# Performance work log

Measured on AMD Instinct MI355X. Metric: run time of the kernel, lower is better.

## Reference

```python
import jax, jax.numpy as jnp
import numpy as np


def setup_inputs() -> dict:
    key = jax.random.key(0)
    k1, k2, k3, k4 = jax.random.split(key, 4)
    B, D_vis, E, N = 512, 4096, 1024, 512
    vf = jax.random.normal(k1, (B, D_vis), dtype=jnp.float32)
    p_lfs = jax.random.normal(k2, (B, E), dtype=jnp.float32)
    n_lfs = jax.random.normal(k3, (N, E), dtype=jnp.float32)
    W = jax.random.normal(k4, (E, D_vis), dtype=jnp.float32) * (1.0 / np.sqrt(D_vis))
    b = jnp.zeros((E,), dtype=jnp.float32)
    return {"vf": vf, "p_lfs": p_lfs, "n_lfs": n_lfs, "W": W, "b": b}


def _partial_order_sim(hypers, hypos):
    # -||relu(hypers - hypos)||_2 along last dim
    act = jax.nn.relu(hypers - hypos)
    return -jnp.sqrt(jnp.sum(act * act, axis=-1))


def reference(vf, p_lfs, n_lfs, W, b):
    # vf: [B, D_vis], W: [E, D_vis] -> vf_emb: [B, E]
    vf_emb = jnp.einsum("bd,ed->be", vf, W) + b
    # positive scores: [B]
    p_scores = _partial_order_sim(p_lfs, vf_emb)
    # negative scores, batched over B: n_lfs [N,E] vs vf_emb [B,E] -> [B,N]
    n_scores = _partial_order_sim(n_lfs[None, :, :], vf_emb[:, None, :])
    # score_stack: [B, 1+N]
    return jnp.concatenate([p_scores[:, None], n_scores], axis=1)
```

## Files before the change

### kernel.cpp

```cpp
#include <hip/hip_runtime.h>
#include <hip/hip_bf16.h>

constexpr int B = 512;
constexpr int D = 4096;
constexpr int E = 1024;
constexpr int N = 512;
constexpr int KS = 8;
constexpr int KC = D / KS;
constexpr int NSTEP = KC / 32;
constexpr int ES = 8;
constexpr int EC = E / ES;
constexpr int DEPTH = 4;

typedef __attribute__((ext_vector_type(8))) short bf16x8;
typedef __attribute__((ext_vector_type(4))) float f32x4;
typedef _Float16 h2 __attribute__((ext_vector_type(2)));
typedef _Float16 h4 __attribute__((ext_vector_type(4)));
typedef _Float16 h8 __attribute__((ext_vector_type(8)));

typedef __attribute__((address_space(3))) void lds_void;
typedef const __attribute__((address_space(1))) void gbl_void;

__device__ __forceinline__ unsigned short f2bf(float f) {
    __hip_bfloat16 h = __float2bfloat16(f);
    return *reinterpret_cast<unsigned short*>(&h);
}

#if __has_builtin(__builtin_amdgcn_fdot2)
__device__ __forceinline__ float fdot2(h2 a, h2 b, float c) {
    return __builtin_amdgcn_fdot2(a, b, c, false);
}
#else
__device__ __forceinline__ float fdot2(h2 a, h2 b, float c) {
    return c + (float)a[0] * (float)b[0] + (float)a[1] * (float)b[1];
}
#endif

__global__ __launch_bounds__(256) void cvt_all(
    const float* __restrict__ vf, const float* __restrict__ W,
    const float* __restrict__ n_lfs,
    unsigned short* __restrict__ vfB, unsigned short* __restrict__ WB,
    _Float16* __restrict__ n16)
{
    const int bid = blockIdx.x;
    if (bid < 3072) {
        const float* src;
        unsigned short* dst;
        int i;
        if (bid < 1024) { src = vf; dst = vfB; i = (bid * 256 + threadIdx.x) * 8; }
        else           { src = W;  dst = WB;  i = ((bid - 1024) * 256 + threadIdx.x) * 8; }
        float4 v0 = *(const float4*)(src + i);
        float4 v1 = *(const float4*)(src + i + 4);
        bf16x8 o;
        o[0] = (short)f2bf(v0.x); o[1] = (short)f2bf(v0.y);
        o[2] = (short)f2bf(v0.z); o[3] = (short)f2bf(v0.w);
        o[4] = (short)f2bf(v1.x); o[5] = (short)f2bf(v1.y);
        o[6] = (short)f2bf(v1.z); o[7] = (short)f2bf(v1.w);
        *(bf16x8*)(dst + i) = o;
    } else {
        const int i = ((bid - 3072) * 256 + threadIdx.x) * 8;
        float4 v0 = *(const float4*)(n_lfs + i);
        float4 v1 = *(const float4*)(n_lfs + i + 4);
        h8 o;
        o[0] = (_Float16)v0.x; o[1] = (_Float16)v0.y;
        o[2] = (_Float16)v0.z; o[3] = (_Float16)v0.w;
        o[4] = (_Float16)v1.x; o[5] = (_Float16)v1.y;
        o[6] = (_Float16)v1.z; o[7] = (_Float16)v1.w;
        *(h8*)(n16 + i) = o;
    }
}

__global__ __launch_bounds__(64) void gemm_lds(
    const unsigned short* __restrict__ vf,
    const unsigned short* __restrict__ W,
    float* __restrict__ part)
{
    __shared__ __align__(16) char smem[32768];

    const int L  = threadIdx.x;

    const int id = blockIdx.x + 16 * blockIdx.y + 128 * blockIdx.z;
    const int l  = (id & 7) * 128 + (id >> 3);
    const int ks = l >> 7;
    const int n0 = (l & 15) * 64;
    const int m0 = ((l >> 4) & 7) * 64;

    const int subrow = L >> 2;
    const int qstg = (L & 3) ^ ((L >> 2) & 3) ^ ((L >> 4) & 3);
    const int kbeg = ks * KC;
    const unsigned short* aSrc[4];
    const unsigned short* bSrc[4];
    #pragma unroll
    for (int c = 0; c < 4; ++c) {
        aSrc[c] = vf + (size_t)(m0 + c * 16 + subrow) * D + kbeg + qstg * 8;
        bSrc[c] = W  + (size_t)(n0 + c * 16 + subrow) * D + kbeg + qstg * 8;
    }

    const int r16 = L & 15;
    const int quad = L >> 4;
    const int swz = quad ^ (r16 & 3) ^ ((r16 >> 2) & 3);
    const int aoff = r16 * 64 + swz * 16;

    f32x4 acc[4][4] = {};

    auto issue = [&](int step, int buf) {
        const size_t koff = (size_t)step * 32;
        #pragma unroll
        for (int c = 0; c < 4; ++c) {
            __builtin_amdgcn_global_load_lds(
                (gbl_void*)(aSrc[c] + koff),
                (lds_void*)(smem + buf * 4096 + c * 1024), 16, 0, 0);
            __builtin_amdgcn_global_load_lds(
                (gbl_void*)(bSrc[c] + koff),
                (lds_void*)(smem + 16384 + buf * 4096 + c * 1024), 16, 0, 0);
        }
    };

    issue(0, 0);
    issue(1, 1);
    issue(2, 2);
    issue(3, 3);

    #define GSTEP(S, WC, ISS)                                                  \
    {                                                                          \
        const int buf_ = (S) & 3;                                              \
        __builtin_amdgcn_s_waitcnt(WC);                                        \
        bf16x8 af[4], bg[4];                                                   \
        _Pragma("unroll")                                                      \
        for (int i = 0; i < 4; ++i)                                            \
            af[i] = *(const bf16x8*)(smem + buf_ * 4096 + i * 1024 + aoff);    \
        _Pragma("unroll")                                                      \
        for (int j = 0; j < 4; ++j)                                            \
            bg[j] = *(const bf16x8*)(smem + 16384 + buf_ * 4096 + j * 1024 + aoff); \
        _Pragma("unroll")                                                      \
        for (int i = 0; i < 4; ++i)                                            \
            _Pragma("unroll")                                                  \
            for (int j = 0; j < 4; ++j)                                        \
                acc[i][j] = __builtin_amdgcn_mfma_f32_16x16x32_bf16(           \
                    af[i], bg[j], acc[i][j], 0, 0, 0);                         \
        if (ISS) issue((S) + DEPTH, buf_);                                     \
    }

    #pragma unroll 1
    for (int s = 0; s < NSTEP - DEPTH; ++s)
        GSTEP(s, 0x4F78, true);
    GSTEP(NSTEP - 4, 0x4F78, false);
    GSTEP(NSTEP - 3, 0x4F70, false);
    GSTEP(NSTEP - 2, 0x0F78, false);
    GSTEP(NSTEP - 1, 0x0F70, false);
    #undef GSTEP

    float* ct = (float*)smem;
    #pragma unroll
    for (int i = 0; i < 4; ++i)
        #pragma unroll
        for (int j = 0; j < 4; ++j)
            #pragma unroll
            for (int r = 0; r < 4; ++r)
                ct[(i * 16 + quad * 4 + r) * 69 + (j * 16 + r16)] = acc[i][j][r];
    __builtin_amdgcn_s_waitcnt(0xC07F);
    __builtin_amdgcn_sched_barrier(0);
    float* po = part + (size_t)ks * B * E + (size_t)(m0 + L) * E + n0;
    const float* crow = ct + L * 69;
    #pragma unroll
    for (int c4 = 0; c4 < 16; ++c4) {
        f32x4 v;
        v[0] = crow[c4 * 4];     v[1] = crow[c4 * 4 + 1];
        v[2] = crow[c4 * 4 + 2]; v[3] = crow[c4 * 4 + 3];
        *(f32x4*)(po + c4 * 4) = v;
    }
}

__global__ __launch_bounds__(256) void reduce_emb(
    const float* __restrict__ part, const float* __restrict__ bias,
    const float* __restrict__ p_lfs,
    _Float16* __restrict__ emb16, float* __restrict__ out)
{
    const int b = blockIdx.x;
    const int e = threadIdx.x * 4;
    const size_t base = (size_t)b * E + e;
    float4 s = *(const float4*)(bias + e);
    #pragma unroll
    for (int ks = 0; ks < KS; ++ks) {
        float4 p = *(const float4*)(part + (size_t)ks * B * E + base);
        s.x += p.x; s.y += p.y; s.z += p.z; s.w += p.w;
    }
    h4 o;
    o[0] = (_Float16)s.x; o[1] = (_Float16)s.y;
    o[2] = (_Float16)s.z; o[3] = (_Float16)s.w;
    *(h4*)(emb16 + base) = o;

    const float4 pl = *(const float4*)(p_lfs + base);
    float d, a = 0.f;
    d = pl.x - s.x; d = fmaxf(d, 0.f); a = fmaf(d, d, a);
    d = pl.y - s.y; d = fmaxf(d, 0.f); a = fmaf(d, d, a);
    d = pl.z - s.z; d = fmaxf(d, 0.f); a = fmaf(d, d, a);
    d = pl.w - s.w; d = fmaxf(d, 0.f); a = fmaf(d, d, a);
    #pragma unroll
    for (int off = 32; off; off >>= 1) a += __shfl_down(a, off, 64);
    __shared__ float red[4];
    if ((threadIdx.x & 63) == 0) red[threadIdx.x >> 6] = a;
    __syncthreads();
    if (threadIdx.x == 0)
        out[(size_t)b * 513] = -sqrtf(red[0] + red[1] + red[2] + red[3]);
}

__global__ __launch_bounds__(256, 4) void scores_part(
    const _Float16* __restrict__ emb16,
    const _Float16* __restrict__ n16,
    float* __restrict__ pn)
{
    constexpr int LDH = EC + 8;
    __shared__ _Float16 eS[64 * LDH];
    __shared__ _Float16 nS[64 * LDH];

    const int t  = threadIdx.x;
    const int n0 = blockIdx.x * 64;
    const int b0 = blockIdx.y * 64;
    const int e0 = blockIdx.z * EC;

    {
        const int row = t >> 2;
        const int cb  = (t & 3) * 32;
        const _Float16* ep = emb16 + (size_t)(b0 + row) * E + e0 + cb;
        const _Float16* np = n16   + (size_t)(n0 + row) * E + e0 + cb;
        _Float16* ed = &eS[row * LDH + cb];
        _Float16* nd = &nS[row * LDH + cb];
        #pragma unroll
        for (int q = 0; q < 4; ++q) {
            h8 v = *(const h8*)(ep + q * 8);
            h8 w = *(const h8*)(np + q * 8);
            *(h8*)(ed + q * 8) = -v;
            *(h8*)(nd + q * 8) = w;
        }
    }
    __syncthreads();

    const int ty = t >> 4;
    const int tx = t & 15;

    float acc[4][4] = {};
    const h4 z4 = {};

    #pragma unroll 2
    for (int e = 0; e < EC; e += 4) {
        h4 a[4], c[4];
        #pragma unroll
        for (int r = 0; r < 4; ++r)
            a[r] = *(const h4*)&eS[(ty + 16 * r) * LDH + e];
        #pragma unroll
        for (int q = 0; q < 4; ++q)
            c[q] = *(const h4*)&nS[(tx + 16 * q) * LDH + e];
        #pragma unroll
        for (int r = 0; r < 4; ++r)
            #pragma unroll
            for (int q = 0; q < 4; ++q) {
                h4 d = c[q] + a[r];
                d = __builtin_elementwise_max(d, z4);
                h2 dl = __builtin_shufflevector(d, d, 0, 1);
                h2 dh = __builtin_shufflevector(d, d, 2, 3);
                acc[r][q] = fdot2(dl, dl, acc[r][q]);
                acc[r][q] = fdot2(dh, dh, acc[r][q]);
            }
    }

    float* po = pn + (size_t)blockIdx.z * B * N;
    #pragma unroll
    for (int r = 0; r < 4; ++r) {
        const size_t ob = (size_t)(b0 + ty + 16 * r) * N;
        #pragma unroll
        for (int q = 0; q < 4; ++q)
            po[ob + n0 + tx + 16 * q] = acc[r][q];
    }
}

__global__ __launch_bounds__(256) void scores_final(
    const float* __restrict__ pn,
    float* __restrict__ out)
{
    const int i = blockIdx.x * 256 + threadIdx.x;
    const int b = i >> 9;
    const int n = i & (N - 1);
    float s = 0.f;
    #pragma unroll
    for (int z = 0; z < ES; ++z)
        s += pn[(size_t)z * B * N + i];
    out[(size_t)b * 513 + 1 + n] = -sqrtf(s);
}

extern "C" void kernel_launch(void* const* d_in, const int* in_sizes, int n_in,
                              void* d_out, int out_size, void* d_ws, size_t ws_size,
                              hipStream_t stream) {
    const float* vf    = (const float*)d_in[0];
    const float* p_lfs = (const float*)d_in[1];
    const float* n_lfs = (const float*)d_in[2];
    const float* W     = (const float*)d_in[3];
    const float* bias  = (const float*)d_in[4];
    float* out = (float*)d_out;

    char* ws = (char*)d_ws;
    float*          pg    = (float*)ws;
    float*          pn    = (float*)ws;
    unsigned short* vfB   = (unsigned short*)(ws + ((size_t)16 << 20));
    unsigned short* WB    = (unsigned short*)(ws + ((size_t)20 << 20));
    _Float16*       emb16 = (_Float16*)(ws + ((size_t)28 << 20));
    _Float16*       n16   = (_Float16*)(ws + ((size_t)29 << 20));

    cvt_all<<<3328, 256, 0, stream>>>(vf, W, n_lfs, vfB, WB, n16);

    dim3 g1(E / 64, B / 64, KS);
    gemm_lds<<<g1, 64, 0, stream>>>(vfB, WB, pg);

    reduce_emb<<<B, 256, 0, stream>>>(pg, bias, p_lfs, emb16, out);

    dim3 g3(N / 64, B / 64, ES);
    scores_part<<<g3, 256, 0, stream>>>(emb16, n16, pn);

    scores_final<<<(B * N) / 256, 256, 0, stream>>>(pn, out);
}
```

Before: 120.7 us.

## Store split-K and score partials in fp16, double split-K, shrink GEMM pipeline

The GEMM split-K factor doubles from 8 to 16, which launches more blocks. The LDS prefetch pipeline drops from 4 stages to 2, cutting shared memory from 32 KB to about 17 KB per block to allow higher occupancy. The GEMM partial embeddings and the per-E-slice score partials are now written and read as fp16 instead of fp32, halving the workspace traffic through the reduction kernels. The cost is a shallower latency-hiding pipeline and extra rounding error in the intermediate partial sums.

After: 118.2 us. 2.1% less time.

```diff
diff --git a/kernel.cpp b/kernel.cpp
--- a/kernel.cpp
+++ b/kernel.cpp
@@ -5,12 +5,12 @@
 constexpr int D = 4096;
 constexpr int E = 1024;
 constexpr int N = 512;
-constexpr int KS = 8;
+constexpr int KS = 16;
 constexpr int KC = D / KS;
 constexpr int NSTEP = KC / 32;
 constexpr int ES = 8;
 constexpr int EC = E / ES;
-constexpr int DEPTH = 4;
+constexpr int DEPTH = 2;
 
 typedef __attribute__((ext_vector_type(8))) short bf16x8;
 typedef __attribute__((ext_vector_type(4))) float f32x4;
@@ -73,14 +73,14 @@
 __global__ __launch_bounds__(64) void gemm_lds(
     const unsigned short* __restrict__ vf,
     const unsigned short* __restrict__ W,
-    float* __restrict__ part)
-{
-    __shared__ __align__(16) char smem[32768];
+    _Float16* __restrict__ part)
+{
+    __shared__ __align__(16) char smem[17664];
 
     const int L  = threadIdx.x;
 
     const int id = blockIdx.x + 16 * blockIdx.y + 128 * blockIdx.z;
-    const int l  = (id & 7) * 128 + (id >> 3);
+    const int l  = (id & 7) * 256 + (id >> 3);
     const int ks = l >> 7;
     const int n0 = (l & 15) * 64;
     const int m0 = ((l >> 4) & 7) * 64;
@@ -112,18 +112,16 @@
                 (lds_void*)(smem + buf * 4096 + c * 1024), 16, 0, 0);
             __builtin_amdgcn_global_load_lds(
                 (gbl_void*)(bSrc[c] + koff),
-                (lds_void*)(smem + 16384 + buf * 4096 + c * 1024), 16, 0, 0);
+                (lds_void*)(smem + 8192 + buf * 4096 + c * 1024), 16, 0, 0);
         }
     };
 
     issue(0, 0);
     issue(1, 1);
-    issue(2, 2);
-    issue(3, 3);
 
     #define GSTEP(S, WC, ISS)                                                  \
     {                                                                          \
-        const int buf_ = (S) & 3;                                              \
+        const int buf_ = (S) & 1;                                              \
         __builtin_amdgcn_s_waitcnt(WC);                                        \
         bf16x8 af[4], bg[4];                                                   \
         _Pragma("unroll")                                                      \
@@ -131,7 +129,7 @@
             af[i] = *(const bf16x8*)(smem + buf_ * 4096 + i * 1024 + aoff);    \
         _Pragma("unroll")                                                      \
         for (int j = 0; j < 4; ++j)                                            \
-            bg[j] = *(const bf16x8*)(smem + 16384 + buf_ * 4096 + j * 1024 + aoff); \
+            bg[j] = *(const bf16x8*)(smem + 8192 + buf_ * 4096 + j * 1024 + aoff); \
         _Pragma("unroll")                                                      \
         for (int i = 0; i < 4; ++i)                                            \
             _Pragma("unroll")                                                  \
@@ -142,11 +140,8 @@
     }
 
     #pragma unroll 1
-    for (int s = 0; s < NSTEP - DEPTH; ++s)
-        GSTEP(s, 0x4F78, true);
-    GSTEP(NSTEP - 4, 0x4F78, false);
-    GSTEP(NSTEP - 3, 0x4F70, false);
-    GSTEP(NSTEP - 2, 0x0F78, false);
+    for (int s = 0; s < NSTEP - 1; ++s)
+        GSTEP(s, 0x0F78, s + DEPTH < NSTEP);
     GSTEP(NSTEP - 1, 0x0F70, false);
     #undef GSTEP
 
@@ -160,19 +155,19 @@
                 ct[(i * 16 + quad * 4 + r) * 69 + (j * 16 + r16)] = acc[i][j][r];
     __builtin_amdgcn_s_waitcnt(0xC07F);
     __builtin_amdgcn_sched_barrier(0);
-    float* po = part + (size_t)ks * B * E + (size_t)(m0 + L) * E + n0;
+    _Float16* po = part + (size_t)ks * B * E + (size_t)(m0 + L) * E + n0;
     const float* crow = ct + L * 69;
     #pragma unroll
-    for (int c4 = 0; c4 < 16; ++c4) {
-        f32x4 v;
-        v[0] = crow[c4 * 4];     v[1] = crow[c4 * 4 + 1];
-        v[2] = crow[c4 * 4 + 2]; v[3] = crow[c4 * 4 + 3];
-        *(f32x4*)(po + c4 * 4) = v;
+    for (int c8 = 0; c8 < 8; ++c8) {
+        h8 v;
+        #pragma unroll
+        for (int u = 0; u < 8; ++u) v[u] = (_Float16)crow[c8 * 8 + u];
+        *(h8*)(po + c8 * 8) = v;
     }
 }
 
 __global__ __launch_bounds__(256) void reduce_emb(
-    const float* __restrict__ part, const float* __restrict__ bias,
+    const _Float16* __restrict__ part, const float* __restrict__ bias,
     const float* __restrict__ p_lfs,
     _Float16* __restrict__ emb16, float* __restrict__ out)
 {
@@ -182,8 +177,9 @@
     float4 s = *(const float4*)(bias + e);
     #pragma unroll
     for (int ks = 0; ks < KS; ++ks) {
-        float4 p = *(const float4*)(part + (size_t)ks * B * E + base);
-        s.x += p.x; s.y += p.y; s.z += p.z; s.w += p.w;
+        h4 p = *(const h4*)(part + (size_t)ks * B * E + base);
+        s.x += (float)p[0]; s.y += (float)p[1];
+        s.z += (float)p[2]; s.w += (float)p[3];
     }
     h4 o;
     o[0] = (_Float16)s.x; o[1] = (_Float16)s.y;
@@ -208,7 +204,7 @@
 __global__ __launch_bounds__(256, 4) void scores_part(
     const _Float16* __restrict__ emb16,
     const _Float16* __restrict__ n16,
-    float* __restrict__ pn)
+    _Float16* __restrict__ pn)
 {
     constexpr int LDH = EC + 8;
     __shared__ _Float16 eS[64 * LDH];
@@ -264,18 +260,18 @@
             }
     }
 
-    float* po = pn + (size_t)blockIdx.z * B * N;
+    _Float16* po = pn + (size_t)blockIdx.z * B * N;
     #pragma unroll
     for (int r = 0; r < 4; ++r) {
         const size_t ob = (size_t)(b0 + ty + 16 * r) * N;
         #pragma unroll
         for (int q = 0; q < 4; ++q)
-            po[ob + n0 + tx + 16 * q] = acc[r][q];
+            po[ob + n0 + tx + 16 * q] = (_Float16)acc[r][q];
     }
 }
 
 __global__ __launch_bounds__(256) void scores_final(
-    const float* __restrict__ pn,
+    const _Float16* __restrict__ pn,
     float* __restrict__ out)
 {
     const int i = blockIdx.x * 256 + threadIdx.x;
@@ -284,7 +280,7 @@
     float s = 0.f;
     #pragma unroll
     for (int z = 0; z < ES; ++z)
-        s += pn[(size_t)z * B * N + i];
+        s += (float)pn[(size_t)z * B * N + i];
     out[(size_t)b * 513 + 1 + n] = -sqrtf(s);
 }
 
@@ -299,8 +295,8 @@
     float* out = (float*)d_out;
 
     char* ws = (char*)d_ws;
-    float*          pg    = (float*)ws;
-    float*          pn    = (float*)ws;
+    _Float16*       pg    = (_Float16*)ws;
+    _Float16*       pn    = (_Float16*)ws;
     unsigned short* vfB   = (unsigned short*)(ws + ((size_t)16 << 20));
     unsigned short* WB    = (unsigned short*)(ws + ((size_t)20 << 20));
     _Float16*       emb16 = (_Float16*)(ws + ((size_t)28 << 20));
```
